# Kernel optimization log

Hardware: AMD Instinct MI355X
Metric: run time of the kernel (lower is better)

The kernel has to match this reference:

```python
import jax, jax.numpy as jnp
import numpy as np

NUM_HEAD = 16
DIM = 1024
T, B = 2048, 4


def setup_inputs() -> dict:
    key = jax.random.key(0)
    ks = jax.random.split(key, 12)
    s = 1.0 / np.sqrt(DIM)
    return {
        "x1": jax.random.normal(ks[0], (T, B, DIM), jnp.float32),
        "x2": jax.random.normal(ks[1], (T, B, DIM), jnp.float32),
        "Wq": jax.random.normal(ks[2], (DIM, DIM), jnp.float32) * s,
        "bq": jax.random.normal(ks[3], (DIM,), jnp.float32) * 0.01,
        "Wk": jax.random.normal(ks[4], (DIM, DIM), jnp.float32) * s,
        "bk": jax.random.normal(ks[5], (DIM,), jnp.float32) * 0.01,
        "Wv": jax.random.normal(ks[6], (DIM, DIM), jnp.float32) * s,
        "bv": jax.random.normal(ks[7], (DIM,), jnp.float32) * 0.01,
        "Wu": jax.random.normal(ks[8], (DIM, DIM), jnp.float32) * s,
        "bu": jax.random.normal(ks[9], (DIM,), jnp.float32) * 0.01,
    }


def reference(x1, x2, Wq, bq, Wk, bk, Wv, bv, Wu, bu):
    T1, B1, C = x1.shape
    T2 = x2.shape[0]
    H = NUM_HEAD
    hd = C // H
    # (T,B,C) -> (B,T,C)
    x1b = jnp.transpose(x1, (1, 0, 2))
    x2b = jnp.transpose(x2, (1, 0, 2))
    # torch Linear: y = x @ W.T + b
    q = (x1b @ Wq.T + bq).reshape(B1, T1, H, hd).transpose(0, 2, 1, 3)  # (B,H,T1,hd)
    k = (x2b @ Wk.T + bk).reshape(B1, T2, H, hd).transpose(0, 2, 1, 3)
    v = (x2b @ Wv.T + bv).reshape(B1, T2, H, hd).transpose(0, 2, 1, 3)
    # NOTE: source scales by 1/sqrt(C) (full dim), not 1/sqrt(head_dim)
    attn = jnp.einsum("bhqd,bhkd->bhqk", q, k) / jnp.sqrt(jnp.asarray(C, q.dtype))
    attn = jax.nn.softmax(attn, axis=-1)
    # dropout = identity (eval mode, deterministic reference)
    out = jnp.einsum("bhqk,bhkd->bhqd", attn, v)  # (B,H,T1,hd)
    out = out.transpose(0, 2, 1, 3).reshape(B1, T1, C)  # merge heads
    out = out @ Wu.T + bu
    return out
```

## Files before the change

kernel.cpp:

```cpp
#include <hip/hip_runtime.h>

#define TSEQ 2048
#define BB 4
#define CDIM 1024
#define NH 16
#define HD 64
#define MR (TSEQ*BB)
#define C2SCALE 0.045084220f

typedef __attribute__((ext_vector_type(8))) short sh8;
typedef __attribute__((ext_vector_type(4))) short sh4;
typedef __attribute__((ext_vector_type(4))) float f4;
typedef __attribute__((ext_vector_type(4))) unsigned int u32x4;

__device__ __forceinline__ unsigned short f2bf(float x){
  unsigned u = __builtin_bit_cast(unsigned, x);
  u += 0x7fffu + ((u>>16)&1u);
  return (unsigned short)(u>>16);
}

__device__ __forceinline__ unsigned cvtpk(float a, float b){
  unsigned r;
  asm("v_cvt_pk_bf16_f32 %0, %1, %2" : "=v"(r) : "v"(a), "v"(b));
  return r;
}

__device__ __forceinline__ void gll16(const unsigned short* g, unsigned short* l){
  __builtin_amdgcn_global_load_lds(
      (const __attribute__((address_space(1))) unsigned int*)g,
      (__attribute__((address_space(3))) unsigned int*)l, 16, 0, 0);
}

__global__ void conv_x(const float* __restrict__ a, const float* __restrict__ b,
                       unsigned short* __restrict__ ya, unsigned short* __restrict__ yb){
  const float* s = blockIdx.y ? b : a;
  unsigned short* d = blockIdx.y ? yb : ya;
  int i = (blockIdx.x*256 + threadIdx.x)*4;
  f4 v = *(const f4*)(s+i);
  sh4 o;
  o.x = (short)f2bf(v.x); o.y = (short)f2bf(v.y);
  o.z = (short)f2bf(v.z); o.w = (short)f2bf(v.w);
  *(sh4*)(d+i) = o;
}

__global__ void conv_w(const float* __restrict__ w0, const float* __restrict__ w1,
                       const float* __restrict__ w2, const float* __restrict__ w3,
                       unsigned short* __restrict__ y0, unsigned short* __restrict__ y1,
                       unsigned short* __restrict__ y2, unsigned short* __restrict__ y3){
  const float* s; unsigned short* d;
  switch(blockIdx.y){
    case 0: s=w0; d=y0; break;
    case 1: s=w1; d=y1; break;
    case 2: s=w2; d=y2; break;
    default: s=w3; d=y3; break;
  }
  int i = (blockIdx.x*256 + threadIdx.x)*4;
  f4 v = *(const f4*)(s+i);
  sh4 o;
  o.x = (short)f2bf(v.x); o.y = (short)f2bf(v.y);
  o.z = (short)f2bf(v.z); o.w = (short)f2bf(v.w);
  *(sh4*)(d+i) = o;
}

#define NKT 16
#define TBUF 32768

__device__ __forceinline__ void gemm_core(
    const unsigned short* __restrict__ Aglob, const unsigned short* __restrict__ Bglob,
    unsigned short* smem, int m0, int n0, int tid, f4 (&acc)[8][4])
{
  const int lane = tid&63;
  const int g = lane>>4, c = lane&15;
  const int wv = tid>>6;
  const int wr = wv>>2, wcn = wv&3;

  const int rloc = tid>>3, cho = tid&7;
  const int aside = (rloc>>5)<<7;
  const int ar = (rloc&31) + aside;
  const int schk = (cho ^ (rloc&7))*8;
  const unsigned short* aS = Aglob + (size_t)(m0+ar)*CDIM + schk;
  const unsigned short* bS = Bglob + (size_t)(n0+rloc)*CDIM + schk;
  const int aD = ar*64 + cho*8;
  const int bD = 16384 + rloc*64 + cho*8;

#define STA(k2,q) gll16(aS + (size_t)(q)*32*CDIM + (k2)*64, smem + ((k2)&1)*TBUF + (q)*2048 + aD)
#define STB(k2,q) gll16(bS + (size_t)(q)*64*CDIM + (k2)*64, smem + ((k2)&1)*TBUF + (q)*4096 + bD)

  const int ch0 = (g ^ (c&7))*8;
  const int ch1 = ((4+g) ^ (c&7))*8;
  const int arow0 = (wr*128 + c)*64;
  const int brow0 = 16384 + (wcn*64 + c)*64;

#pragma unroll
  for (int q=0;q<4;q++) STA(0,q);
#pragma unroll
  for (int q=0;q<4;q++) STB(0,q);
#pragma unroll
  for (int q=0;q<3;q++){ STA(1,q); STB(1,q); }
  asm volatile("s_waitcnt vmcnt(6)" ::: "memory");
  __builtin_amdgcn_s_barrier();

  for (int kt=0; kt<NKT; kt++){
    const unsigned short* bufA = smem + (kt&1)*TBUF;
    sh8 bfr[4][2];
#pragma unroll
    for (int p=0; p<4; p++){
      sh8 af[2][2];
#pragma unroll
      for (int i=0;i<2;i++){
        af[i][0] = *(const sh8*)(bufA + arow0 + (2*p+i)*1024 + ch0);
        af[i][1] = *(const sh8*)(bufA + arow0 + (2*p+i)*1024 + ch1);
      }
      if (p==0){
#pragma unroll
        for (int nt=0;nt<4;nt++){
          bfr[nt][0] = *(const sh8*)(bufA + brow0 + nt*1024 + ch0);
          bfr[nt][1] = *(const sh8*)(bufA + brow0 + nt*1024 + ch1);
        }
      }
      if (p==0){
        if (kt+1 < NKT){ STA(kt+1,3); STB(kt+1,3); }
      } else {
        if (kt+2 < NKT){ STA(kt+2,p-1); STB(kt+2,p-1); }
      }
      __builtin_amdgcn_s_barrier();
      __builtin_amdgcn_s_setprio(1);
#pragma unroll
      for (int i=0;i<2;i++)
#pragma unroll
        for (int nt=0;nt<4;nt++){
          acc[2*p+i][nt] = __builtin_amdgcn_mfma_f32_16x16x32_bf16(af[i][0], bfr[nt][0], acc[2*p+i][nt],0,0,0);
          acc[2*p+i][nt] = __builtin_amdgcn_mfma_f32_16x16x32_bf16(af[i][1], bfr[nt][1], acc[2*p+i][nt],0,0,0);
        }
      __builtin_amdgcn_s_setprio(0);
      if (p==3){
        if (kt < NKT-2)       asm volatile("s_waitcnt vmcnt(6)" ::: "memory");
        else if (kt == NKT-2) asm volatile("s_waitcnt vmcnt(0)" ::: "memory");
      }
      __builtin_amdgcn_s_barrier();
    }
  }
#undef STA
#undef STB
}

__global__ __launch_bounds__(512,2) void gemm_u(
    const unsigned short* __restrict__ A, const unsigned short* __restrict__ Bw,
    const float* __restrict__ bias, float* __restrict__ Cout){
  __shared__ unsigned short smem[2*TBUF];
  const int tid  = threadIdx.x;
  const int lane = tid&63;
  const int g = lane>>4, c = lane&15;
  const int wv = tid>>6;
  const int wr = wv>>2, wcn = wv&3;
  const int m0 = blockIdx.x*256, n0 = blockIdx.y*256;
  f4 acc[8][4] = {};
  gemm_core(A, Bw, smem, m0, n0, tid, acc);

#pragma unroll
  for (int nt=0; nt<4; nt++){
    int nn = n0 + wcn*64 + nt*16 + c;
    float bsv = bias[nn];
#pragma unroll
    for (int mt=0; mt<8; mt++){
      int mb = m0 + wr*128 + mt*16 + 4*g;
#pragma unroll
      for (int r=0; r<4; r++)
        Cout[(size_t)(mb+r)*CDIM + nn] = acc[mt][nt][r] + bsv;
    }
  }
}

__global__ __launch_bounds__(512,2) void gemm_qkv(
    const unsigned short* __restrict__ x1b, const unsigned short* __restrict__ x2b,
    const unsigned short* __restrict__ wq, const unsigned short* __restrict__ wk,
    const unsigned short* __restrict__ wv,
    const float* __restrict__ bq, const float* __restrict__ bk, const float* __restrict__ bv,
    unsigned short* __restrict__ Qo, unsigned short* __restrict__ Ko,
    unsigned short* __restrict__ Vo){
  __shared__ unsigned short smem[2*TBUF];
  const int z = blockIdx.z;
  const unsigned short* A  = (z==0) ? x1b : x2b;
  const unsigned short* Bw = (z==0) ? wq : (z==1) ? wk : wv;
  const float* bias        = (z==0) ? bq : (z==1) ? bk : bv;
  const int tid  = threadIdx.x;
  const int lane = tid&63;
  const int g = lane>>4, c = lane&15;
  const int wv2 = tid>>6;
  const int wr = wv2>>2, wcn = wv2&3;
  const int m0 = blockIdx.x*256, n0 = blockIdx.y*256;
  f4 acc[8][4] = {};
  gemm_core(A, Bw, smem, m0, n0, tid, acc);

#pragma unroll
  for (int nt=0; nt<4; nt++){
    int nn = n0 + wcn*64 + nt*16 + c;
    float bsv = bias[nn];
#pragma unroll
    for (int mt=0; mt<8; mt++){
      int mb = m0 + wr*128 + mt*16 + 4*g;
#pragma unroll
      for (int r=0; r<4; r++){
        float v = acc[mt][nt][r] + bsv;
        int mm = mb + r;
        if (z==0){
          Qo[(size_t)mm*CDIM + nn] = f2bf(v*C2SCALE);
        } else if (z==1){
          Ko[(size_t)mm*CDIM + nn] = f2bf(v);
        } else {
          int t = mm>>2, bb = mm&3, h = nn>>6, d = nn&63;
          Vo[(((size_t)bb*NH + h)*HD + d)*TSEQ + t] = f2bf(v);
        }
      }
    }
  }
}

__global__ __launch_bounds__(256,4) void attn_kernel(
    const unsigned short* __restrict__ Q, const unsigned short* __restrict__ Kb,
    const unsigned short* __restrict__ Vt, unsigned short* __restrict__ O){
  __shared__ unsigned short Ks[2][64*64];
  __shared__ unsigned short Vs[2][64*64];
  const int tid=threadIdx.x, wave=tid>>6, lane=tid&63;
  const int g=lane>>4, c=lane&15;
  const bool godd = (g&1);
  const int gx = blockIdx.x;
  const int bh = ((gx>>7)<<3) | (gx&7);
  const int qt = (gx>>3)&15;
  const int b = bh>>4, h = bh&15;
  const int qbase = qt*128 + wave*32;

  const unsigned short* kb0[2];
  const unsigned short* vb0[2];
#pragma unroll
  for (int i=0; i<2; i++){
    int cc = i*256+tid;
    int krow = cc>>3, kch = (cc&7) ^ (krow&7);
    kb0[i] = Kb + ((size_t)krow*BB + b)*CDIM + h*HD + kch*8;
    int vd = cc>>3, vch = (cc&7) ^ (vd&7);
    vb0[i] = Vt + ((size_t)(b*NH+h)*HD + vd)*TSEQ + vch*8;
  }

  sh8 qfr[2][2];
#pragma unroll
  for (int qf=0; qf<2; qf++)
#pragma unroll
    for (int kc=0; kc<2; kc++){
      int t = qbase + qf*16 + c;
      qfr[qf][kc] = *(const sh8*)(Q + ((size_t)t*BB + b)*CDIM + h*HD + kc*32 + g*8);
    }

  f4 oacc[4][2] = {};
  float lrun[2] = {0.f, 0.f};

#pragma unroll
  for (int i=0; i<2; i++){
    gll16(kb0[i], Ks[0] + (i*256+tid)*8);
    gll16(vb0[i], Vs[0] + (i*256+tid)*8);
  }
  __syncthreads();

  const int NT = TSEQ/64;
  int cur = 0;
  for (int it=0; it<NT; it++){
    if (it+1 < NT){
      int k0n = (it+1)*64;
#pragma unroll
      for (int i=0; i<2; i++){
        gll16(kb0[i] + (size_t)k0n*BB*CDIM, Ks[cur^1] + (i*256+tid)*8);
        gll16(vb0[i] + k0n,                 Vs[cur^1] + (i*256+tid)*8);
      }
    }
    const unsigned short* ks = Ks[cur];
    const unsigned short* vs = Vs[cur];

#pragma unroll
    for (int sub=0; sub<2; sub++){
      f4 sacc[2][2] = {};
      __builtin_amdgcn_s_setprio(1);
#pragma unroll
      for (int j=0; j<2; j++){
        int kf = sub*2 + j;
        sh8 af[2];
#pragma unroll
        for (int kc=0; kc<2; kc++){
          int ch = (kc*4+g) ^ (c&7);
          af[kc] = *(const sh8*)(ks + (kf*16+c)*64 + ch*8);
        }
#pragma unroll
        for (int kc=0; kc<2; kc++)
#pragma unroll
          for (int qf=0; qf<2; qf++)
            sacc[j][qf] = __builtin_amdgcn_mfma_f32_16x16x32_bf16(af[kc], qfr[qf][kc], sacc[j][qf],0,0,0);
      }
      __builtin_amdgcn_s_setprio(0);

      sh8 pf[2];
#pragma unroll
      for (int qf=0; qf<2; qf++){
        f4 sa = sacc[0][qf];
        f4 sb = sacc[1][qf];
        float pa0 = __builtin_amdgcn_exp2f(sa[0]);
        float pa1 = __builtin_amdgcn_exp2f(sa[1]);
        float pa2 = __builtin_amdgcn_exp2f(sa[2]);
        float pa3 = __builtin_amdgcn_exp2f(sa[3]);
        float pb0 = __builtin_amdgcn_exp2f(sb[0]);
        float pb1 = __builtin_amdgcn_exp2f(sb[1]);
        float pb2 = __builtin_amdgcn_exp2f(sb[2]);
        float pb3 = __builtin_amdgcn_exp2f(sb[3]);
        lrun[qf] += ((pa0+pa1)+(pa2+pa3)) + ((pb0+pb1)+(pb2+pb3));
        unsigned A0 = cvtpk(pa0, pa1);
        unsigned A1 = cvtpk(pa2, pa3);
        unsigned B0 = cvtpk(pb0, pb1);
        unsigned B1 = cvtpk(pb2, pb3);
        asm("v_permlane32_swap_b32 %0, %1" : "+v"(A0), "+v"(B0));
        asm("v_permlane32_swap_b32 %0, %1" : "+v"(A1), "+v"(B1));
        unsigned xA0 = (unsigned)__builtin_amdgcn_ds_swizzle((int)A0, 0x401F);
        unsigned xA1 = (unsigned)__builtin_amdgcn_ds_swizzle((int)A1, 0x401F);
        unsigned xB0 = (unsigned)__builtin_amdgcn_ds_swizzle((int)B0, 0x401F);
        unsigned xB1 = (unsigned)__builtin_amdgcn_ds_swizzle((int)B1, 0x401F);
        u32x4 pw;
        pw.x = godd ? xB0 : A0;
        pw.y = godd ? xB1 : A1;
        pw.z = godd ? B0  : xA0;
        pw.w = godd ? B1  : xA1;
        pf[qf] = __builtin_bit_cast(sh8, pw);
      }
      __builtin_amdgcn_s_setprio(1);
#pragma unroll
      for (int df=0; df<4; df++){
        int ch = (sub*4+g) ^ (c&7);
        sh8 vf = *(const sh8*)(vs + (df*16+c)*64 + ch*8);
#pragma unroll
        for (int qf=0; qf<2; qf++)
          oacc[df][qf] = __builtin_amdgcn_mfma_f32_16x16x32_bf16(vf, pf[qf], oacc[df][qf],0,0,0);
      }
      __builtin_amdgcn_s_setprio(0);
    }

    __syncthreads();
    cur ^= 1;
  }

#pragma unroll
  for (int qf=0; qf<2; qf++){
    lrun[qf] += __shfl_xor(lrun[qf], 16, 64);
    lrun[qf] += __shfl_xor(lrun[qf], 32, 64);
    float inv = 1.0f/lrun[qf];
    int t = qbase + qf*16 + c;
#pragma unroll
    for (int df=0; df<4; df++){
      uint2 pr;
      pr.x = cvtpk(oacc[df][qf][0]*inv, oacc[df][qf][1]*inv);
      pr.y = cvtpk(oacc[df][qf][2]*inv, oacc[df][qf][3]*inv);
      *(uint2*)(O + ((size_t)b*TSEQ + t)*CDIM + h*HD + df*16 + 4*g) = pr;
    }
  }
}

extern "C" void kernel_launch(void* const* d_in, const int* in_sizes, int n_in,
                              void* d_out, int out_size, void* d_ws, size_t ws_size,
                              hipStream_t stream){
  (void)in_sizes; (void)n_in; (void)out_size; (void)ws_size;
  const float* x1 = (const float*)d_in[0];
  const float* x2 = (const float*)d_in[1];
  const float* Wq = (const float*)d_in[2];
  const float* bq = (const float*)d_in[3];
  const float* Wk = (const float*)d_in[4];
  const float* bk = (const float*)d_in[5];
  const float* Wv = (const float*)d_in[6];
  const float* bv = (const float*)d_in[7];
  const float* Wu = (const float*)d_in[8];
  const float* bu = (const float*)d_in[9];

  unsigned short* ws = (unsigned short*)d_ws;
  size_t o = 0;
  unsigned short* x1b = ws + o; o += (size_t)MR*CDIM;
  unsigned short* x2b = ws + o; o += (size_t)MR*CDIM;
  unsigned short* wqb = ws + o; o += (size_t)CDIM*CDIM;
  unsigned short* wkb = ws + o; o += (size_t)CDIM*CDIM;
  unsigned short* wvb = ws + o; o += (size_t)CDIM*CDIM;
  unsigned short* wub = ws + o; o += (size_t)CDIM*CDIM;
  unsigned short* Qb  = ws + o; o += (size_t)MR*CDIM;
  unsigned short* Kbf = ws + o; o += (size_t)MR*CDIM;
  unsigned short* Vtb = ws + o; o += (size_t)MR*CDIM;
  unsigned short* Ob  = x1b;

  conv_x<<<dim3((MR*CDIM)/1024, 2),   256, 0, stream>>>(x1, x2, x1b, x2b);
  conv_w<<<dim3((CDIM*CDIM)/1024, 4), 256, 0, stream>>>(Wq, Wk, Wv, Wu, wqb, wkb, wvb, wub);

  gemm_qkv<<<dim3(MR/256, CDIM/256, 3), 512, 0, stream>>>(
      x1b, x2b, wqb, wkb, wvb, bq, bk, bv, Qb, Kbf, Vtb);
  attn_kernel<<<dim3(1024), 256, 0, stream>>>(Qb, Kbf, Vtb, Ob);
  gemm_u<<<dim3(MR/256, CDIM/256), 512, 0, stream>>>(Ob, wub, bu, (float*)d_out);
}
```

Baseline: 333.4 us.

## Retile output projection GEMM and stage V transpose through shared memory

The output projection GEMM gets a new core that uses 256x128 tiles, 4 waves, a 3-stage LDS ring buffer and one block per CU, which doubles the grid to 256 blocks for better CU coverage. The V-projection epilogue now writes bias-added bf16 values into swizzled shared memory, then stores transposed V rows as 16-byte vectors instead of scattered 2-byte stores. Together these aim to cut under-occupancy in the final GEMM and uncoalesced writes in the QKV epilogue. The risks are more A-tile reloads in the U GEMM and an extra barrier plus LDS round trip in the V path.

```diff
diff --git a/kernel.cpp b/kernel.cpp
--- a/kernel.cpp
+++ b/kernel.cpp
@@ -62,10 +62,108 @@
   *(sh4*)(d+i) = o;
 }
 
+#define NKT4 16
+#define BUFS4 24576
+
+__device__ __forceinline__ void gemm_core4(
+    const unsigned short* __restrict__ Aglob, const unsigned short* __restrict__ Bglob,
+    unsigned short* smem, int m0, int n0, int tid, f4 (&acc)[8][4])
+{
+  const int wave = tid>>6, lane = tid&63;
+  const int g = lane>>4, c = lane&15;
+  const int wr = wave>>1, wc = wave&1;
+
+  const int srow = tid>>3, sch = tid&7;
+  const unsigned short* aBase = Aglob + (size_t)(m0+srow)*CDIM + (sch^(srow&7))*8;
+  const unsigned short* bBase = Bglob + (size_t)(n0+srow)*CDIM + (sch^(srow&7))*8;
+
+#pragma unroll
+  for (int i=0;i<8;i++) gll16(aBase + (size_t)i*32*CDIM,      smem + (i*256+tid)*8);
+#pragma unroll
+  for (int i=0;i<4;i++) gll16(bBase + (size_t)i*32*CDIM,      smem + 16384 + (i*256+tid)*8);
+#pragma unroll
+  for (int i=0;i<8;i++) gll16(aBase + (size_t)i*32*CDIM + 64, smem + BUFS4 + (i*256+tid)*8);
+#pragma unroll
+  for (int i=0;i<4;i++) gll16(bBase + (size_t)i*32*CDIM + 64, smem + BUFS4 + 16384 + (i*256+tid)*8);
+  asm volatile("s_waitcnt vmcnt(12)" ::: "memory");
+  __builtin_amdgcn_s_barrier();
+
+  const int arow = wr*128 + c;
+  const int brow = wc*64 + c;
+  const int ch0 = g ^ (c&7);
+  const int ch1 = (4+g) ^ (c&7);
+
+  int q = 0;
+  for (int kt=0; kt<NKT4; kt++){
+    unsigned short* bufc = smem + q*BUFS4;
+    int rr = q+2; if (rr>=3) rr-=3;
+    unsigned short* dst = smem + rr*BUFS4;
+    if (kt+2 < NKT4){
+      const size_t koff = (size_t)(kt+2)*64;
+#pragma unroll
+      for (int i=0;i<8;i++) gll16(aBase + (size_t)i*32*CDIM + koff, dst + (i*256+tid)*8);
+#pragma unroll
+      for (int i=0;i<4;i++) gll16(bBase + (size_t)i*32*CDIM + koff, dst + 16384 + (i*256+tid)*8);
+    }
+    sh8 af[8][2], bfr[4][2];
+#pragma unroll
+    for (int mt=0;mt<8;mt++){
+      af[mt][0] = *(const sh8*)(bufc + (arow+mt*16)*64 + ch0*8);
+      af[mt][1] = *(const sh8*)(bufc + (arow+mt*16)*64 + ch1*8);
+    }
+#pragma unroll
+    for (int nt=0;nt<4;nt++){
+      bfr[nt][0] = *(const sh8*)(bufc + 16384 + (brow+nt*16)*64 + ch0*8);
+      bfr[nt][1] = *(const sh8*)(bufc + 16384 + (brow+nt*16)*64 + ch1*8);
+    }
+    __builtin_amdgcn_s_setprio(1);
+#pragma unroll
+    for (int mt=0;mt<8;mt++)
+#pragma unroll
+      for (int nt=0;nt<4;nt++){
+        acc[mt][nt] = __builtin_amdgcn_mfma_f32_16x16x32_bf16(af[mt][0], bfr[nt][0], acc[mt][nt],0,0,0);
+        acc[mt][nt] = __builtin_amdgcn_mfma_f32_16x16x32_bf16(af[mt][1], bfr[nt][1], acc[mt][nt],0,0,0);
+      }
+    __builtin_amdgcn_s_setprio(0);
+    if (kt < NKT4-1){
+      if (kt < NKT4-2) asm volatile("s_waitcnt vmcnt(12)" ::: "memory");
+      else             asm volatile("s_waitcnt vmcnt(0)" ::: "memory");
+    }
+    __builtin_amdgcn_s_barrier();
+    q = (q==2)?0:q+1;
+  }
+}
+
+__global__ __launch_bounds__(256,1) void gemm_u(
+    const unsigned short* __restrict__ A, const unsigned short* __restrict__ Bw,
+    const float* __restrict__ bias, float* __restrict__ Cout){
+  __shared__ unsigned short smem[3*BUFS4];
+  const int tid  = threadIdx.x;
+  const int wave = tid>>6, lane = tid&63;
+  const int g = lane>>4, c = lane&15;
+  const int m0 = blockIdx.x*256, n0 = blockIdx.y*128;
+  const int wr = wave>>1, wc = wave&1;
+  f4 acc[8][4] = {};
+  gemm_core4(A, Bw, smem, m0, n0, tid, acc);
+
+#pragma unroll
+  for (int nt=0; nt<4; nt++){
+    int nn = n0 + wc*64 + nt*16 + c;
+    float bsv = bias[nn];
+#pragma unroll
+    for (int mt=0; mt<8; mt++){
+      int mb = m0 + wr*128 + mt*16 + 4*g;
+#pragma unroll
+      for (int r=0; r<4; r++)
+        Cout[(size_t)(mb+r)*CDIM + nn] = acc[mt][nt][r] + bsv;
+    }
+  }
+}
+
 #define NKT 16
 #define TBUF 32768
 
-__device__ __forceinline__ void gemm_core(
+__device__ __forceinline__ void gemm_core8(
     const unsigned short* __restrict__ Aglob, const unsigned short* __restrict__ Bglob,
     unsigned short* smem, int m0, int n0, int tid, f4 (&acc)[8][4])
 {
@@ -142,33 +240,6 @@
   }
 #undef STA
 #undef STB
-}
-
-__global__ __launch_bounds__(512,2) void gemm_u(
-    const unsigned short* __restrict__ A, const unsigned short* __restrict__ Bw,
-    const float* __restrict__ bias, float* __restrict__ Cout){
-  __shared__ unsigned short smem[2*TBUF];
-  const int tid  = threadIdx.x;
-  const int lane = tid&63;
-  const int g = lane>>4, c = lane&15;
-  const int wv = tid>>6;
-  const int wr = wv>>2, wcn = wv&3;
-  const int m0 = blockIdx.x*256, n0 = blockIdx.y*256;
-  f4 acc[8][4] = {};
-  gemm_core(A, Bw, smem, m0, n0, tid, acc);
-
-#pragma unroll
-  for (int nt=0; nt<4; nt++){
-    int nn = n0 + wcn*64 + nt*16 + c;
-    float bsv = bias[nn];
-#pragma unroll
-    for (int mt=0; mt<8; mt++){
-      int mb = m0 + wr*128 + mt*16 + 4*g;
-#pragma unroll
-      for (int r=0; r<4; r++)
-        Cout[(size_t)(mb+r)*CDIM + nn] = acc[mt][nt][r] + bsv;
-    }
-  }
 }
 
 __global__ __launch_bounds__(512,2) void gemm_qkv(
@@ -190,28 +261,50 @@
   const int wr = wv2>>2, wcn = wv2&3;
   const int m0 = blockIdx.x*256, n0 = blockIdx.y*256;
   f4 acc[8][4] = {};
-  gemm_core(A, Bw, smem, m0, n0, tid, acc);
-
-#pragma unroll
-  for (int nt=0; nt<4; nt++){
-    int nn = n0 + wcn*64 + nt*16 + c;
-    float bsv = bias[nn];
-#pragma unroll
-    for (int mt=0; mt<8; mt++){
-      int mb = m0 + wr*128 + mt*16 + 4*g;
-#pragma unroll
-      for (int r=0; r<4; r++){
-        float v = acc[mt][nt][r] + bsv;
-        int mm = mb + r;
-        if (z==0){
-          Qo[(size_t)mm*CDIM + nn] = f2bf(v*C2SCALE);
-        } else if (z==1){
-          Ko[(size_t)mm*CDIM + nn] = f2bf(v);
-        } else {
-          int t = mm>>2, bb = mm&3, h = nn>>6, d = nn&63;
-          Vo[(((size_t)bb*NH + h)*HD + d)*TSEQ + t] = f2bf(v);
+  gemm_core8(A, Bw, smem, m0, n0, tid, acc);
+
+  if (z != 2){
+#pragma unroll
+    for (int nt=0; nt<4; nt++){
+      int nn = n0 + wcn*64 + nt*16 + c;
+      float bsv = bias[nn];
+#pragma unroll
+      for (int mt=0; mt<8; mt++){
+        int mb = m0 + wr*128 + mt*16 + 4*g;
+#pragma unroll
+        for (int r=0; r<4; r++){
+          float v = acc[mt][nt][r] + bsv;
+          int mm = mb + r;
+          if (z==0) Qo[(size_t)mm*CDIM + nn] = f2bf(v*C2SCALE);
+          else      Ko[(size_t)mm*CDIM + nn] = f2bf(v);
         }
       }
+    }
+  } else {
+    unsigned short* lv = smem;
+#pragma unroll
+    for (int nt=0; nt<4; nt++){
+      int nl = wcn*64 + nt*16 + c;
+      float bsv = bias[n0 + nl];
+      int key = (nl&7)<<3;
+#pragma unroll
+      for (int mt=0; mt<8; mt++){
+        int tl = wr*32 + mt*4 + g;
+        int pos = nl*256 + (tl ^ key);
+#pragma unroll
+        for (int r=0; r<4; r++)
+          lv[pos + r*64] = f2bf(acc[mt][nt][r] + bsv);
+      }
+    }
+    __builtin_amdgcn_s_barrier();
+    const int j = tid&7;
+#pragma unroll
+    for (int it=0; it<16; it++){
+      int rid = it*64 + (tid>>3);
+      int nl = rid>>2, bb = rid&3;
+      sh8 vrow = *(const sh8*)(lv + nl*256 + bb*64 + ((j ^ (nl&7))<<3));
+      int nn = n0 + nl; int h = nn>>6, d = nn&63;
+      *(sh8*)(Vo + ((size_t)(bb*NH + h)*HD + d)*TSEQ + (m0>>2) + j*8) = vrow;
     }
   }
 }
@@ -392,5 +485,5 @@
   gemm_qkv<<<dim3(MR/256, CDIM/256, 3), 512, 0, stream>>>(
       x1b, x2b, wqb, wkb, wvb, bq, bk, bv, Qb, Kbf, Vtb);
   attn_kernel<<<dim3(1024), 256, 0, stream>>>(Qb, Kbf, Vtb, Ob);
-  gemm_u<<<dim3(MR/256, CDIM/256), 512, 0, stream>>>(Ob, wub, bu, (float*)d_out);
-}
+  gemm_u<<<dim3(MR/256, CDIM/128), 256, 0, stream>>>(Ob, wub, bu, (float*)d_out);
+}
```

After: 308.5 us. -7.5%, faster.
